# Kernel tuning notes

Hardware: AMD Instinct MI355X
Metric: run time of the kernel (lower is better)

## Reference

```python
import jax, jax.numpy as jnp
import numpy as np

B, T, D, N = 16, 4096, 512, 3


def _window_sum(x, k):
    # x: [B, T, ...] -> sliding-window sum of size k, stride 1 -> [B, T-k+1, ...]
    c = jnp.cumsum(x, axis=1)
    c = jnp.concatenate([jnp.zeros_like(c[:, :1]), c], axis=1)
    return c[:, k:] - c[:, :-k]


def setup_inputs() -> dict:
    key = jax.random.key(0)
    ks = jax.random.split(key, 7)
    s_prev = jax.random.normal(ks[0], (B, D), jnp.float32)
    enc_hs = jax.random.normal(ks[1], (B, T, D), jnp.float32)
    # realistic padding mask: True = padded position
    lengths = jax.random.randint(ks[2], (B,), T // 2, T + 1)
    src_mask = jnp.arange(T)[None, :] >= lengths[:, None]
    scale = 1.0 / np.sqrt(D)
    Vw = jax.random.normal(ks[3], (N, D, D), jnp.float32) * scale
    Vb = jax.random.normal(ks[4], (N, D), jnp.float32) * 0.01
    Ww = jax.random.normal(ks[5], (N, D, D), jnp.float32) * scale
    Wb = jax.random.normal(ks[6], (N, D), jnp.float32) * 0.01
    return {"s_prev": s_prev, "enc_hs": enc_hs, "src_mask": src_mask,
            "Vw": Vw, "Vb": Vb, "Ww": Ww, "Wb": Wb}


def _level(s_prev, hs, mask, vw, vb, ww, wb):
    # hs: [B, L, D], mask: [B, L] (True = masked)
    # torch Linear: y = x @ W^T + b, weight is [out, in]
    v = jnp.einsum('bld,ed->ble', hs, vw) + vb            # V_i(hs)
    att = jnp.einsum('bd,bld->bl', s_prev, v)             # bmm(s_prev, V(hs)^T)
    att = jnp.where(mask, -jnp.inf, att)
    att = jax.nn.softmax(att, axis=-1)                    # [B, L]
    pooled = jnp.einsum('bl,bld->bd', att, hs)            # bmm(att, hs)
    ctx = pooled @ ww.T + wb                              # W_i(.)
    return ctx, att


def reference(s_prev, enc_hs, src_mask, Vw, Vb, Ww, Wb):
    ctx, att = _level(s_prev, enc_hs, src_mask, Vw[0], Vb[0], Ww[0], Wb[0])
    for i in range(1, N):
        k = i + 1
        hs_ngram = _window_sum(enc_hs, k) / k                      # AvgPool1d(k,1)
        n_mask = _window_sum(src_mask.astype(jnp.float32), k) > 0  # any masked in window
        c, _ = _level(s_prev, hs_ngram, n_mask, Vw[i], Vb[i], Ww[i], Wb[i])
        ctx = ctx + c
    return ctx, att
```

## Files before the change

### kernel.cpp

```cpp
#include <hip/hip_runtime.h>

#define BB 16
#define TT 4096
#define DD 512
#define CH 64
#define NY (TT/CH)
#define NEG (-1.0e30f)

#define OFF_Q     64
#define OFF_P0    (OFF_Q + 3*BB*DD)
#define OFF_M     (OFF_P0 + BB*TT)
#define OFF_S     (OFF_M + 3*BB*NY)
#define OFF_MT    (OFF_S + 3*BB*NY)
#define OFF_TOT   (OFF_MT + 64)
#define OFF_PART  (OFF_TOT + 64)
#define OFF_POOL  (OFF_PART + 3*NY*BB*DD)

__global__ void __launch_bounds__(256) k_lengths(const unsigned char* __restrict__ mask,
                                                 int* __restrict__ lengths) {
    __shared__ int sflag;
    __shared__ int wsum[4];
    const int tid = threadIdx.x;
    const int b = blockIdx.x;
    if (tid == 0) sflag = 0;
    __syncthreads();
    const uint4* m4 = (const uint4*)mask;
    int f = 0;
    #pragma unroll 4
    for (int idx = tid; idx < BB * TT / 16; idx += 256) {
        const uint4 w = m4[idx];
        f |= (((w.x | w.y | w.z | w.w) & 0xFFFFFF00u) != 0u);
    }
    if (f) atomicOr(&sflag, 1);
    __syncthreads();
    const bool byte_layout = (sflag != 0);
    const int* m32 = (const int*)mask;
    int cnt = 0;
    if (byte_layout) {
        for (int t = tid; t < TT; t += 256) cnt += (mask[b * TT + t] != 0);
    } else {
        for (int t = tid; t < TT; t += 256) cnt += (m32[b * TT + t] != 0);
    }
    #pragma unroll
    for (int m = 32; m >= 1; m >>= 1) cnt += __shfl_xor(cnt, m, 64);
    if ((tid & 63) == 0) wsum[tid >> 6] = cnt;
    __syncthreads();
    if (tid == 0) lengths[b] = TT - (wsum[0] + wsum[1] + wsum[2] + wsum[3]);
}

__global__ void __launch_bounds__(1024) k_q(const float* __restrict__ s_prev,
                                            const float* __restrict__ Vw,
                                            float* __restrict__ q) {
    __shared__ float red[4][DD];
    const int ib = blockIdx.x;
    const int b = ib % BB;
    const int i = ib / BB;
    const int ec = threadIdx.x >> 8;
    const int d0 = threadIdx.x & 255;
    const float* sp = s_prev + b * DD + ec * 128;
    const float* W = Vw + (size_t)i * DD * DD + (size_t)(ec * 128) * DD;
    float a0 = 0.f, a1 = 0.f;
    #pragma unroll 4
    for (int e = 0; e < 128; e++) {
        const float se = sp[e];
        a0 += se * W[e * DD + d0];
        a1 += se * W[e * DD + d0 + 256];
    }
    red[ec][d0] = a0;
    red[ec][d0 + 256] = a1;
    __syncthreads();
    if (threadIdx.x < DD)
        q[(size_t)ib * DD + threadIdx.x] = red[0][threadIdx.x] + red[1][threadIdx.x]
                                         + red[2][threadIdx.x] + red[3][threadIdx.x];
}

__global__ void __launch_bounds__(512, 4) k_fused(const float* __restrict__ enc,
                                                  const float* __restrict__ q,
                                                  const int* __restrict__ lengths,
                                                  float* __restrict__ p0,
                                                  float* __restrict__ mbuf,
                                                  float* __restrict__ sbuf,
                                                  float* __restrict__ part) {
    __shared__ float sp[CH + 2][3];
    __shared__ float su[3][CH];
    const int b = blockIdx.x;
    const int y = blockIdx.y;
    const int t0 = y * CH;
    const int len = lengths[b];
    const int tid = threadIdx.x;
    if (t0 >= len) {
        if (tid < 3) {
            mbuf[(size_t)(tid * BB + b) * NY + y] = NEG;
            sbuf[(size_t)(tid * BB + b) * NY + y] = 0.f;
        }
        return;
    }
    const int wv = tid >> 6, lane = tid & 63;

    const float4* q40 = (const float4*)(q + (size_t)(0 * BB + b) * DD);
    const float4* q41 = (const float4*)(q + (size_t)(1 * BB + b) * DD);
    const float4* q42 = (const float4*)(q + (size_t)(2 * BB + b) * DD);
    const float4 qa0 = q40[lane], qb0 = q40[64 + lane];
    const float4 qa1 = q41[lane], qb1 = q41[64 + lane];
    const float4 qa2 = q42[lane], qb2 = q42[64 + lane];

    auto row_task = [&](const int r, const bool wp0) {
        const int t = t0 + r;
        float d0 = 0.f, d1 = 0.f, d2 = 0.f;
        if (t < len) {
            const float4* e4 = (const float4*)(enc + ((size_t)b * TT + t) * DD);
            const float4 x0 = e4[lane], x1 = e4[64 + lane];
            d0 = x0.x*qa0.x + x0.y*qa0.y + x0.z*qa0.z + x0.w*qa0.w
               + x1.x*qb0.x + x1.y*qb0.y + x1.z*qb0.z + x1.w*qb0.w;
            d1 = x0.x*qa1.x + x0.y*qa1.y + x0.z*qa1.z + x0.w*qa1.w
               + x1.x*qb1.x + x1.y*qb1.y + x1.z*qb1.z + x1.w*qb1.w;
            d2 = x0.x*qa2.x + x0.y*qa2.y + x0.z*qa2.z + x0.w*qa2.w
               + x1.x*qb2.x + x1.y*qb2.y + x1.z*qb2.z + x1.w*qb2.w;
            #pragma unroll
            for (int m = 32; m >= 1; m >>= 1) {
                d0 += __shfl_xor(d0, m, 64);
                d1 += __shfl_xor(d1, m, 64);
                d2 += __shfl_xor(d2, m, 64);
            }
        }
        if (lane == 0) {
            sp[r][0] = d0; sp[r][1] = d1; sp[r][2] = d2;
            if (wp0 && t < len) p0[(size_t)b * TT + t] = d0;
        }
    };
    #pragma unroll 2
    for (int rr = 0; rr < 8; rr++) row_task(wv + rr * 8, true);
    if (wv < 2) row_task(CH + wv, false);
    __syncthreads();

    if (tid < 192) {
        const int i = wv;
        const int r = lane;
        const int l = t0 + r;
        const bool valid = l < (len - i);
        float s = sp[r][i];
        if (i > 0) s += sp[r + 1][i];
        if (i > 1) s += sp[r + 2][i];
        const float kin = (i == 0) ? 1.0f : ((i == 1) ? 0.5f : (1.0f / 3.0f));
        const float v = valid ? s * kin : NEG;
        float m = v;
        #pragma unroll
        for (int mm = 32; mm >= 1; mm >>= 1) m = fmaxf(m, __shfl_xor(m, mm, 64));
        const float u = valid ? __expf(v - m) : 0.f;
        su[i][r] = u;
        float ts = u;
        #pragma unroll
        for (int mm = 32; mm >= 1; mm >>= 1) ts += __shfl_xor(ts, mm, 64);
        if (r == 0) {
            mbuf[(size_t)(i * BB + b) * NY + y] = m;
            sbuf[(size_t)(i * BB + b) * NY + y] = ts;
        }
    }
    __syncthreads();

    const float* col = enc + (size_t)b * TT * DD + tid;
    float va = col[(size_t)t0 * DD];
    float vb2 = (t0 + 1 < TT) ? col[(size_t)(t0 + 1) * DD] : 0.f;
    float a0 = 0.f, a1 = 0.f, a2 = 0.f;
    #pragma unroll 16
    for (int rr = 0; rr < CH; rr++) {
        const int t = t0 + rr;
        const float vc = (t + 2 < TT) ? col[(size_t)(t + 2) * DD] : 0.f;
        const float u0 = su[0][rr], u1 = su[1][rr], u2 = su[2][rr];
        const float w1 = va + vb2;
        const float w2 = w1 + vc;
        a0 += u0 * va;
        a1 += u1 * w1;
        a2 += u2 * w2;
        va = vb2; vb2 = vc;
    }
    a1 *= 0.5f; a2 *= (1.0f / 3.0f);
    float* pt = part + (size_t)y * BB * DD + (size_t)b * DD + tid;
    pt[0] = a0;
    pt[(size_t)NY * BB * DD] = a1;
    pt[(size_t)2 * NY * BB * DD] = a2;
}

__global__ void __launch_bounds__(256) k_reduce(const float* __restrict__ part,
                                                const float* __restrict__ mbuf,
                                                const float* __restrict__ sbuf,
                                                float* __restrict__ pooled,
                                                float* __restrict__ mtot,
                                                float* __restrict__ tot) {
    __shared__ float ssc[NY];
    const int blk = blockIdx.x;
    const int ib = blk >> 1;
    const int d = ((blk & 1) << 8) + threadIdx.x;
    const int i = ib / BB, b = ib % BB;
    if (threadIdx.x < 64) {
        const int lane = threadIdx.x;
        const float ml = mbuf[(size_t)ib * NY + lane];
        const float sl = sbuf[(size_t)ib * NY + lane];
        float m = ml;
        #pragma unroll
        for (int s = 32; s >= 1; s >>= 1) m = fmaxf(m, __shfl_xor(m, s, 64));
        float t = sl * __expf(ml - m);
        #pragma unroll
        for (int s = 32; s >= 1; s >>= 1) t += __shfl_xor(t, s, 64);
        ssc[lane] = __expf(ml - m) / t;
        if (lane == 0 && (blk & 1) == 0) { mtot[ib] = m; tot[ib] = t; }
    }
    __syncthreads();
    const float* base = part + (size_t)i * NY * BB * DD + (size_t)b * DD + d;
    float s = 0.f;
    #pragma unroll 8
    for (int yy = 0; yy < NY; yy++) s += base[(size_t)yy * BB * DD] * ssc[yy];
    pooled[(size_t)ib * DD + d] = s;
}

__global__ void __launch_bounds__(256) k_out(const float* __restrict__ pooled,
                                             const float* __restrict__ Ww,
                                             const float* __restrict__ Wb,
                                             const float* __restrict__ p0,
                                             const int* __restrict__ lengths,
                                             const float* __restrict__ mtot,
                                             const float* __restrict__ tot,
                                             float* __restrict__ ctx,
                                             float* __restrict__ att) {
    if (blockIdx.x < BB * DD / 4) {
        const int wid = blockIdx.x * 4 + (threadIdx.x >> 6);
        const int lane = threadIdx.x & 63;
        const int b = wid >> 9;
        const int e = wid & 511;
        float acc = 0.f;
        #pragma unroll
        for (int i = 0; i < 3; i++) {
            const float4* pr = (const float4*)(pooled + (size_t)(i * BB + b) * DD);
            const float4* wr = (const float4*)(Ww + ((size_t)i * DD + e) * DD);
            const float4 pA = pr[lane], pB = pr[64 + lane];
            const float4 wA = wr[lane], wB = wr[64 + lane];
            acc += pA.x * wA.x + pA.y * wA.y + pA.z * wA.z + pA.w * wA.w
                 + pB.x * wB.x + pB.y * wB.y + pB.z * wB.z + pB.w * wB.w;
        }
        #pragma unroll
        for (int m = 32; m >= 1; m >>= 1) acc += __shfl_xor(acc, m, 64);
        if (lane == 0)
            ctx[(size_t)b * DD + e] = acc + Wb[e] + Wb[DD + e] + Wb[2 * DD + e];
    } else {
        const int idx = (blockIdx.x - BB * DD / 4) * 256 + threadIdx.x;
        const int b = idx >> 12;
        const int t = idx & (TT - 1);
        att[idx] = (t < lengths[b]) ? __expf(p0[idx] - mtot[b]) * (1.0f / tot[b]) : 0.f;
    }
}

extern "C" void kernel_launch(void* const* d_in, const int* in_sizes, int n_in,
                              void* d_out, int out_size, void* d_ws, size_t ws_size,
                              hipStream_t stream) {
    const float* s_prev = (const float*)d_in[0];
    const float* enc    = (const float*)d_in[1];
    const void*  mask   = d_in[2];
    const float* Vw     = (const float*)d_in[3];
    const float* Ww     = (const float*)d_in[5];
    const float* Wb     = (const float*)d_in[6];

    float* out = (float*)d_out;
    float* ctx = out;
    float* att = out + BB * DD;

    float* W       = (float*)d_ws;
    int*   lengths = (int*)d_ws;
    float* q       = W + OFF_Q;
    float* p0      = W + OFF_P0;
    float* mbuf    = W + OFF_M;
    float* sbuf    = W + OFF_S;
    float* mtot    = W + OFF_MT;
    float* tot     = W + OFF_TOT;
    float* part    = W + OFF_PART;
    float* pooled  = W + OFF_POOL;

    k_lengths<<<BB, 256, 0, stream>>>((const unsigned char*)mask, lengths);
    k_q<<<48, 1024, 0, stream>>>(s_prev, Vw, q);
    k_fused<<<dim3(BB, NY), 512, 0, stream>>>(enc, q, lengths, p0, mbuf, sbuf, part);
    k_reduce<<<96, 256, 0, stream>>>(part, mbuf, sbuf, pooled, mtot, tot);
    k_out<<<BB * DD / 4 + BB * TT / 256, 256, 0, stream>>>(pooled, Ww, Wb, p0, lengths,
                                                           mtot, tot, ctx, att);
}
```

Before: 255.9 us.

## Stage encoder chunk in shared memory and halve chunk size for reuse

The fused kernel now stores each chunk of encoder rows (plus two halo rows) in shared memory during the dot-product pass. The weighted-pooling pass then reads from LDS instead of re-reading those rows column-wise from global memory, so each block reads enc from HBM once instead of twice. The chunk size drops from 64 to 32 so the 34x512 float LDS tile (about 70 KB) fits, which doubles the grid and the number of partial results. The reduce kernel is adjusted to merge 128 partials per row. Rows past the padded length are now loaded and computed anyway, and the larger LDS footprint may limit occupancy.

```diff
diff --git a/kernel.cpp b/kernel.cpp
--- a/kernel.cpp
+++ b/kernel.cpp
@@ -3,7 +3,7 @@
 #define BB 16
 #define TT 4096
 #define DD 512
-#define CH 64
+#define CH 32
 #define NY (TT/CH)
 #define NEG (-1.0e30f)
 
@@ -81,6 +81,7 @@
                                                   float* __restrict__ mbuf,
                                                   float* __restrict__ sbuf,
                                                   float* __restrict__ part) {
+    __shared__ float se[CH + 2][DD];
     __shared__ float sp[CH + 2][3];
     __shared__ float su[3][CH];
     const int b = blockIdx.x;
@@ -106,73 +107,84 @@
 
     auto row_task = [&](const int r, const bool wp0) {
         const int t = t0 + r;
-        float d0 = 0.f, d1 = 0.f, d2 = 0.f;
-        if (t < len) {
+        float4 x0 = make_float4(0.f, 0.f, 0.f, 0.f), x1 = x0;
+        if (t < TT) {
             const float4* e4 = (const float4*)(enc + ((size_t)b * TT + t) * DD);
-            const float4 x0 = e4[lane], x1 = e4[64 + lane];
-            d0 = x0.x*qa0.x + x0.y*qa0.y + x0.z*qa0.z + x0.w*qa0.w
-               + x1.x*qb0.x + x1.y*qb0.y + x1.z*qb0.z + x1.w*qb0.w;
-            d1 = x0.x*qa1.x + x0.y*qa1.y + x0.z*qa1.z + x0.w*qa1.w
-               + x1.x*qb1.x + x1.y*qb1.y + x1.z*qb1.z + x1.w*qb1.w;
-            d2 = x0.x*qa2.x + x0.y*qa2.y + x0.z*qa2.z + x0.w*qa2.w
-               + x1.x*qb2.x + x1.y*qb2.y + x1.z*qb2.z + x1.w*qb2.w;
-            #pragma unroll
-            for (int m = 32; m >= 1; m >>= 1) {
-                d0 += __shfl_xor(d0, m, 64);
-                d1 += __shfl_xor(d1, m, 64);
-                d2 += __shfl_xor(d2, m, 64);
-            }
+            x0 = e4[lane]; x1 = e4[64 + lane];
+        }
+        ((float4*)se[r])[lane] = x0;
+        ((float4*)se[r])[64 + lane] = x1;
+        float d0 = x0.x*qa0.x + x0.y*qa0.y + x0.z*qa0.z + x0.w*qa0.w
+                 + x1.x*qb0.x + x1.y*qb0.y + x1.z*qb0.z + x1.w*qb0.w;
+        float d1 = x0.x*qa1.x + x0.y*qa1.y + x0.z*qa1.z + x0.w*qa1.w
+                 + x1.x*qb1.x + x1.y*qb1.y + x1.z*qb1.z + x1.w*qb1.w;
+        float d2 = x0.x*qa2.x + x0.y*qa2.y + x0.z*qa2.z + x0.w*qa2.w
+                 + x1.x*qb2.x + x1.y*qb2.y + x1.z*qb2.z + x1.w*qb2.w;
+        #pragma unroll
+        for (int m = 32; m >= 1; m >>= 1) {
+            d0 += __shfl_xor(d0, m, 64);
+            d1 += __shfl_xor(d1, m, 64);
+            d2 += __shfl_xor(d2, m, 64);
         }
         if (lane == 0) {
             sp[r][0] = d0; sp[r][1] = d1; sp[r][2] = d2;
-            if (wp0 && t < len) p0[(size_t)b * TT + t] = d0;
+            if (wp0 && t < TT) p0[(size_t)b * TT + t] = d0;
         }
     };
-    #pragma unroll 2
-    for (int rr = 0; rr < 8; rr++) row_task(wv + rr * 8, true);
+    #pragma unroll
+    for (int rr = 0; rr < 4; rr++) row_task(wv + rr * 8, true);
     if (wv < 2) row_task(CH + wv, false);
     __syncthreads();
 
     if (tid < 192) {
         const int i = wv;
-        const int r = lane;
+        const bool act = lane < CH;
+        const int r = lane & (CH - 1);
         const int l = t0 + r;
-        const bool valid = l < (len - i);
-        float s = sp[r][i];
-        if (i > 0) s += sp[r + 1][i];
-        if (i > 1) s += sp[r + 2][i];
-        const float kin = (i == 0) ? 1.0f : ((i == 1) ? 0.5f : (1.0f / 3.0f));
-        const float v = valid ? s * kin : NEG;
+        const bool valid = act && (l < (len - i));
+        float v = NEG;
+        if (act) {
+            float s = sp[r][i];
+            if (i > 0) s += sp[r + 1][i];
+            if (i > 1) s += sp[r + 2][i];
+            const float kin = (i == 0) ? 1.0f : ((i == 1) ? 0.5f : (1.0f / 3.0f));
+            v = valid ? s * kin : NEG;
+        }
         float m = v;
         #pragma unroll
         for (int mm = 32; mm >= 1; mm >>= 1) m = fmaxf(m, __shfl_xor(m, mm, 64));
         const float u = valid ? __expf(v - m) : 0.f;
-        su[i][r] = u;
+        if (act) su[i][r] = u;
         float ts = u;
         #pragma unroll
         for (int mm = 32; mm >= 1; mm >>= 1) ts += __shfl_xor(ts, mm, 64);
-        if (r == 0) {
+        if (lane == 0) {
             mbuf[(size_t)(i * BB + b) * NY + y] = m;
             sbuf[(size_t)(i * BB + b) * NY + y] = ts;
         }
     }
     __syncthreads();
 
-    const float* col = enc + (size_t)b * TT * DD + tid;
-    float va = col[(size_t)t0 * DD];
-    float vb2 = (t0 + 1 < TT) ? col[(size_t)(t0 + 1) * DD] : 0.f;
+    float va = se[0][tid], vb2 = se[1][tid];
     float a0 = 0.f, a1 = 0.f, a2 = 0.f;
-    #pragma unroll 16
-    for (int rr = 0; rr < CH; rr++) {
-        const int t = t0 + rr;
-        const float vc = (t + 2 < TT) ? col[(size_t)(t + 2) * DD] : 0.f;
-        const float u0 = su[0][rr], u1 = su[1][rr], u2 = su[2][rr];
-        const float w1 = va + vb2;
-        const float w2 = w1 + vc;
-        a0 += u0 * va;
-        a1 += u1 * w1;
-        a2 += u2 * w2;
-        va = vb2; vb2 = vc;
+    #pragma unroll
+    for (int g = 0; g < CH / 4; g++) {
+        const float4 U0 = *(const float4*)&su[0][g * 4];
+        const float4 U1 = *(const float4*)&su[1][g * 4];
+        const float4 U2 = *(const float4*)&su[2][g * 4];
+        const float u0a[4] = {U0.x, U0.y, U0.z, U0.w};
+        const float u1a[4] = {U1.x, U1.y, U1.z, U1.w};
+        const float u2a[4] = {U2.x, U2.y, U2.z, U2.w};
+        #pragma unroll
+        for (int j = 0; j < 4; j++) {
+            const float vc = se[g * 4 + j + 2][tid];
+            const float w1 = va + vb2;
+            const float w2 = w1 + vc;
+            a0 += u0a[j] * va;
+            a1 += u1a[j] * w1;
+            a2 += u2a[j] * w2;
+            va = vb2; vb2 = vc;
+        }
     }
     a1 *= 0.5f; a2 *= (1.0f / 3.0f);
     float* pt = part + (size_t)y * BB * DD + (size_t)b * DD + tid;
@@ -194,15 +206,25 @@
     const int i = ib / BB, b = ib % BB;
     if (threadIdx.x < 64) {
         const int lane = threadIdx.x;
-        const float ml = mbuf[(size_t)ib * NY + lane];
-        const float sl = sbuf[(size_t)ib * NY + lane];
-        float m = ml;
+        float ml[2], sl[2];
+        float m = NEG;
+        #pragma unroll
+        for (int j = 0; j < 2; j++) {
+            ml[j] = mbuf[(size_t)ib * NY + lane * 2 + j];
+            sl[j] = sbuf[(size_t)ib * NY + lane * 2 + j];
+            m = fmaxf(m, ml[j]);
+        }
         #pragma unroll
         for (int s = 32; s >= 1; s >>= 1) m = fmaxf(m, __shfl_xor(m, s, 64));
-        float t = sl * __expf(ml - m);
+        float t = 0.f;
+        #pragma unroll
+        for (int j = 0; j < 2; j++) t += sl[j] * __expf(ml[j] - m);
         #pragma unroll
         for (int s = 32; s >= 1; s >>= 1) t += __shfl_xor(t, s, 64);
-        ssc[lane] = __expf(ml - m) / t;
+        const float inv = 1.0f / t;
+        #pragma unroll
+        for (int j = 0; j < 2; j++)
+            ssc[lane * 2 + j] = __expf(ml[j] - m) * inv;
         if (lane == 0 && (blk & 1) == 0) { mtot[ib] = m; tot[ib] = t; }
     }
     __syncthreads();
```

After: 251.3 us. About the same (-1.8%).
